# Performance work log

Measured on AMD Instinct MI355X. Metric: run time of the kernel, lower is better.

Reference implementation:

```python
import jax, jax.numpy as jnp
import numpy as np

UNITS = 256

def _lstm_step(carry, idx, kernel, rec_kernel, bias, num_chars):
    h, c = carry
    x = jax.nn.one_hot(idx, num_chars, dtype=h.dtype)          # [B, num_chars]
    z = x @ kernel + h @ rec_kernel + bias                      # [B, 4*UNITS]
    i, f, g, o = jnp.split(z, 4, axis=-1)                       # Keras gate order i,f,c,o
    i = jax.nn.sigmoid(i)
    f = jax.nn.sigmoid(f)
    g = jnp.tanh(g)
    o = jax.nn.sigmoid(o)
    c_new = f * c + i * g
    h_new = o * jnp.tanh(c_new)
    return (h_new, c_new), None


def setup_inputs() -> dict:
    key = jax.random.key(0)
    ks = jax.random.split(key, 4)
    num_chars, batch, seq_len = 128, 1024, 512
    x = jax.random.randint(ks[0], (batch, seq_len), 0, num_chars, dtype=jnp.int32)
    kernel = jax.random.normal(ks[1], (num_chars, 4 * UNITS), dtype=jnp.float32) * 0.05
    rec_kernel = jax.random.normal(ks[2], (UNITS, 4 * UNITS), dtype=jnp.float32) * 0.05
    bias = jnp.zeros((4 * UNITS,), dtype=jnp.float32)
    dense_w = jax.random.normal(ks[3], (UNITS, num_chars), dtype=jnp.float32) * 0.05
    dense_b = jnp.zeros((num_chars,), dtype=jnp.float32)
    return {"x": x, "kernel": kernel, "rec_kernel": rec_kernel, "bias": bias,
            "dense_w": dense_w, "dense_b": dense_b}


def reference(x, kernel, rec_kernel, bias, dense_w, dense_b):
    batch = x.shape[0]
    num_chars = kernel.shape[0]
    h0 = jnp.zeros((batch, UNITS), dtype=kernel.dtype)
    c0 = jnp.zeros((batch, UNITS), dtype=kernel.dtype)
    step = lambda carry, idx: _lstm_step(carry, idx, kernel, rec_kernel, bias, num_chars)
    (h, _), _ = jax.lax.scan(step, (h0, c0), x.T)  # scan over time: [S, B]
    logits = h @ dense_w + dense_b                  # [B, num_chars]
    return jax.nn.softmax(logits, axis=-1)
```

## Files before the change

kernel.cpp:

```cpp
#include <hip/hip_runtime.h>
#include <cstdint>

typedef __bf16 bf16x8 __attribute__((ext_vector_type(8)));
typedef float  f32x4  __attribute__((ext_vector_type(4)));

union U4B { uint4 u; bf16x8 b; };
__device__ __forceinline__ bf16x8 as_bf(uint4 u) { U4B x; x.u = u; return x.b; }

__device__ __forceinline__ unsigned short f2b(float x) {
  unsigned int u = __float_as_uint(x);
  unsigned int r = (u + 0x7fffu + ((u >> 16) & 1u)) >> 16;
  return (unsigned short)r;
}
__device__ __forceinline__ float b2f(unsigned int bits_lo16) {
  return __uint_as_float(bits_lo16 << 16);
}

__device__ __forceinline__ float sigm(float x) {
  float e = __builtin_amdgcn_exp2f(x * -1.4426950408889634f);
  return __builtin_amdgcn_rcpf(1.0f + e);
}
__device__ __forceinline__ float tanh_fast(float x) {
  float e = __builtin_amdgcn_exp2f(x * 2.8853900817779268f);
  return 1.0f - 2.0f * __builtin_amdgcn_rcpf(e + 1.0f);
}

__global__ void prep_kernel(const float* __restrict__ rec,
                            const float* __restrict__ kern,
                            const float* __restrict__ bias,
                            const float* __restrict__ dw,
                            unsigned short* __restrict__ recT,
                            unsigned short* __restrict__ kb2,
                            unsigned short* __restrict__ dwT) {
  int id = blockIdx.x * 256 + threadIdx.x;
  if (id < 262144) {
    int colp = id >> 8, k = id & 255;
    int u = colp >> 2, g = colp & 3;
    recT[colp * 256 + k] = f2b(rec[k * 1024 + u + 256 * g]);
  } else if (id < 262144 + 131072) {
    int i = id - 262144;
    int ch = i >> 10, colp = i & 1023;
    int u = colp >> 2, g = colp & 3;
    int oc = u + 256 * g;
    kb2[ch * 1024 + colp] = f2b(kern[ch * 1024 + oc] + bias[oc]);
  } else {
    int i = id - 262144 - 131072;
    int cls = i >> 8, k = i & 255;
    dwT[cls * 256 + k] = f2b(dw[k * 128 + cls]);
  }
}

__global__ __launch_bounds__(512)
__attribute__((amdgpu_waves_per_eu(2, 2)))
void lstm_kernel(
    const unsigned short* __restrict__ recT,
    const unsigned short* __restrict__ kb2,
    const unsigned short* __restrict__ dwT,
    const int* __restrict__ x,
    const float* __restrict__ dense_b,
    float* __restrict__ out) {
  __shared__ uint4 A_lds[2][8][512];
  __shared__ unsigned short h_buf[2][16][264];

  const int tid   = threadIdx.x;
  const int lane  = tid & 63;
  const int wid   = tid >> 6;
  const int row16 = lane & 15;
  const int kg    = lane >> 4;
  const int rbase = blockIdx.x << 4;

  const unsigned short* recBase = recT + ((wid * 128 + row16) * 256 + kg * 8);

  uint4 af[4][8];
#pragma unroll
  for (int m = 0; m < 4; ++m)
#pragma unroll
    for (int k = 0; k < 8; ++k) {
      af[m][k] = *(const uint4*)(recBase + m * 4096 + k * 32);
      asm volatile("" : "+a"(af[m][k].x), "+a"(af[m][k].y),
                        "+a"(af[m][k].z), "+a"(af[m][k].w));
    }

#pragma unroll
  for (int s = 0; s < 2; ++s)
#pragma unroll
    for (int k = 0; k < 8; ++k)
      A_lds[s][k][wid * 64 + lane] = *(const uint4*)(recBase + (4 + s) * 4096 + k * 32);

  const unsigned short* sb6 = recBase + 6 * 4096;
  const unsigned short* sb7 = recBase + 7 * 4096;
  uint4 st6[8], st7[8];
#pragma unroll
  for (int k = 0; k < 4; ++k) {
    st6[k] = *(const uint4*)(sb6 + k * 32);
    st7[k] = *(const uint4*)(sb7 + k * 32);
  }

  for (int e = tid; e < 16 * 264; e += 512) (&h_buf[0][0][0])[e] = 0;

  float c_state[8];
#pragma unroll
  for (int m = 0; m < 8; ++m) c_state[m] = 0.0f;

  const int* xrow = x + (rbase + row16) * 512;
  int idx_cur = xrow[0];
  const int colb = wid * 128;

  uint2 kq0[4], kq1[4];
  {
    const unsigned short* kb = kb2 + (idx_cur * 1024 + colb + kg * 4);
#pragma unroll
    for (int m = 0; m < 4; ++m) { kq0[m] = *(const uint2*)(kb + m * 16);
                                  kq1[m] = *(const uint2*)(kb + (4 + m) * 16); }
  }

  __syncthreads();

  int cur = 0;
  const unsigned aoff_base = (wid * 64 + lane) * 16;

#pragma unroll 1
  for (int t = 0; t < 512; ++t) {
    unsigned z6 = 0, zL = 0;
    asm volatile("" : "+v"(z6), "+v"(zL));
    const unsigned short* sb6v = sb6 + z6;
    const unsigned short* sb7v = sb7 + z6;
    const unsigned aoff = aoff_base + zL;

#pragma unroll
    for (int k = 4; k < 8; ++k) {
      st6[k] = *(const uint4*)(sb6v + k * 32);
      st7[k] = *(const uint4*)(sb7v + k * 32);
    }
    int idx_next = xrow[(t + 1 < 512) ? t + 1 : 511];

    const unsigned short* hrow = &h_buf[cur][row16][0];
    unsigned short* hn = &h_buf[cur ^ 1][row16][wid * 32 + kg];

    f32x4 a0 = {0,0,0,0}, a1 = {0,0,0,0}, a2 = {0,0,0,0}, a3 = {0,0,0,0};
#pragma unroll
    for (int k = 0; k < 8; ++k) {
      uint4 hf = *(const uint4*)(hrow + k * 32 + kg * 8);
      a0 = __builtin_amdgcn_mfma_f32_16x16x32_bf16(as_bf(af[0][k]), as_bf(hf), a0, 0, 0, 0);
      a1 = __builtin_amdgcn_mfma_f32_16x16x32_bf16(as_bf(af[1][k]), as_bf(hf), a1, 0, 0, 0);
      a2 = __builtin_amdgcn_mfma_f32_16x16x32_bf16(as_bf(af[2][k]), as_bf(hf), a2, 0, 0, 0);
      a3 = __builtin_amdgcn_mfma_f32_16x16x32_bf16(as_bf(af[3][k]), as_bf(hf), a3, 0, 0, 0);
    }
    {
      f32x4 ag[4] = {a0, a1, a2, a3};
#pragma unroll
      for (int m = 0; m < 4; ++m) {
        float zi = ag[m][0] + b2f(kq0[m].x & 0xffffu);
        float zf = ag[m][1] + b2f(kq0[m].x >> 16);
        float zg = ag[m][2] + b2f(kq0[m].y & 0xffffu);
        float zo = ag[m][3] + b2f(kq0[m].y >> 16);
        float c  = sigm(zf) * c_state[m] + sigm(zi) * tanh_fast(zg);
        c_state[m] = c;
        hn[m * 4] = f2b(sigm(zo) * tanh_fast(c));
      }
    }

    const unsigned short* kbn = kb2 + (idx_next * 1024 + colb + kg * 4);
#pragma unroll
    for (int m = 0; m < 4; ++m) kq0[m] = *(const uint2*)(kbn + m * 16);

    f32x4 b0 = {0,0,0,0}, b1 = {0,0,0,0}, b2v = {0,0,0,0}, b3 = {0,0,0,0};
#pragma unroll
    for (int k = 0; k < 8; ++k) {
      uint4 hf = *(const uint4*)(hrow + k * 32 + kg * 8);
      uint4 a4 = *(const uint4*)((const char*)A_lds + (0 * 8 + k) * 8192 + aoff);
      uint4 a5 = *(const uint4*)((const char*)A_lds + (1 * 8 + k) * 8192 + aoff);
      b0 = __builtin_amdgcn_mfma_f32_16x16x32_bf16(as_bf(a4), as_bf(hf), b0, 0, 0, 0);
      b1 = __builtin_amdgcn_mfma_f32_16x16x32_bf16(as_bf(a5), as_bf(hf), b1, 0, 0, 0);
      b2v = __builtin_amdgcn_mfma_f32_16x16x32_bf16(as_bf(st6[k]), as_bf(hf), b2v, 0, 0, 0);
      b3 = __builtin_amdgcn_mfma_f32_16x16x32_bf16(as_bf(st7[k]), as_bf(hf), b3, 0, 0, 0);
      if (k < 4) {
        st6[k] = *(const uint4*)(sb6v + k * 32);
        st7[k] = *(const uint4*)(sb7v + k * 32);
      }
    }
    {
      f32x4 bg[4] = {b0, b1, b2v, b3};
#pragma unroll
      for (int m = 0; m < 4; ++m) {
        float zi = bg[m][0] + b2f(kq1[m].x & 0xffffu);
        float zf = bg[m][1] + b2f(kq1[m].x >> 16);
        float zg = bg[m][2] + b2f(kq1[m].y & 0xffffu);
        float zo = bg[m][3] + b2f(kq1[m].y >> 16);
        float c  = sigm(zf) * c_state[4 + m] + sigm(zi) * tanh_fast(zg);
        c_state[4 + m] = c;
        hn[(4 + m) * 4] = f2b(sigm(zo) * tanh_fast(c));
      }
    }

#pragma unroll
    for (int m = 0; m < 4; ++m) kq1[m] = *(const uint2*)(kbn + (4 + m) * 16);

    __syncthreads();
    cur ^= 1;
    idx_cur = idx_next;
  }

  float (*l_lds)[132] = (float (*)[132])A_lds;
  {
    const unsigned short* dwBase = dwT + ((wid * 16 + row16) * 256 + kg * 8);
    f32x4 la = {0.f, 0.f, 0.f, 0.f};
#pragma unroll
    for (int k = 0; k < 8; ++k) {
      uint4 hf  = *(const uint4*)&h_buf[0][row16][k * 32 + kg * 8];
      uint4 afd = *(const uint4*)(dwBase + k * 32);
      la = __builtin_amdgcn_mfma_f32_16x16x32_bf16(as_bf(afd), as_bf(hf), la, 0, 0, 0);
    }
#pragma unroll
    for (int r = 0; r < 4; ++r) {
      int cls = wid * 16 + kg * 4 + r;
      l_lds[row16][cls] = la[r] + dense_b[cls];
    }
  }
  __syncthreads();

  {
    int r = tid >> 5, cg = tid & 31;
    float4 v = *(const float4*)&l_lds[r][cg * 4];
    float mx = fmaxf(fmaxf(v.x, v.y), fmaxf(v.z, v.w));
#pragma unroll
    for (int sh = 1; sh < 32; sh <<= 1) mx = fmaxf(mx, __shfl_xor(mx, sh));
    const float L2E = 1.4426950408889634f;
    float e0 = __builtin_amdgcn_exp2f((v.x - mx) * L2E);
    float e1 = __builtin_amdgcn_exp2f((v.y - mx) * L2E);
    float e2 = __builtin_amdgcn_exp2f((v.z - mx) * L2E);
    float e3 = __builtin_amdgcn_exp2f((v.w - mx) * L2E);
    float sm = e0 + e1 + e2 + e3;
#pragma unroll
    for (int sh = 1; sh < 32; sh <<= 1) sm += __shfl_xor(sm, sh);
    float inv = __builtin_amdgcn_rcpf(sm);
    float4 o = {e0 * inv, e1 * inv, e2 * inv, e3 * inv};
    *(float4*)&out[(rbase + r) * 128 + cg * 4] = o;
  }
}

extern "C" void kernel_launch(void* const* d_in, const int* in_sizes, int n_in,
                              void* d_out, int out_size, void* d_ws, size_t ws_size,
                              hipStream_t stream) {
  const int*   x      = (const int*)d_in[0];
  const float* kern   = (const float*)d_in[1];
  const float* rec    = (const float*)d_in[2];
  const float* bias   = (const float*)d_in[3];
  const float* dw     = (const float*)d_in[4];
  const float* db     = (const float*)d_in[5];
  float* outp = (float*)d_out;

  unsigned char* ws = (unsigned char*)d_ws;
  unsigned short* recT = (unsigned short*)(ws);
  unsigned short* kb2  = (unsigned short*)(ws + 524288);
  unsigned short* dwT  = (unsigned short*)(ws + 786432);

  prep_kernel<<<1664, 256, 0, stream>>>(rec, kern, bias, dw, recT, kb2, dwT);
  lstm_kernel<<<64, 512, 0, stream>>>(recT, kb2, dwT, x, db, outp);
}
```

Measured before the change: 2.784 ms.

## Permute hidden-unit K order so each lane writes h as one 16-byte store

```diff
diff --git a/kernel.cpp b/kernel.cpp
--- a/kernel.cpp
+++ b/kernel.cpp
@@ -23,6 +23,10 @@
 __device__ __forceinline__ float tanh_fast(float x) {
   float e = __builtin_amdgcn_exp2f(x * 2.8853900817779268f);
   return 1.0f - 2.0f * __builtin_amdgcn_rcpf(e + 1.0f);
+}
+
+__device__ __forceinline__ int kperm_u(int k) {
+  return (k & ~31) + (k & 7) * 4 + ((k >> 3) & 3);
 }
 
 __global__ void prep_kernel(const float* __restrict__ rec,
@@ -35,18 +39,19 @@
   int id = blockIdx.x * 256 + threadIdx.x;
   if (id < 262144) {
     int colp = id >> 8, k = id & 255;
-    int u = colp >> 2, g = colp & 3;
-    recT[colp * 256 + k] = f2b(rec[k * 1024 + u + 256 * g]);
+    int u = kperm_u(k);
+    int oc = (colp >> 2) + 256 * (colp & 3);
+    recT[colp * 256 + k] = f2b(rec[u * 1024 + oc]);
   } else if (id < 262144 + 131072) {
     int i = id - 262144;
     int ch = i >> 10, colp = i & 1023;
-    int u = colp >> 2, g = colp & 3;
-    int oc = u + 256 * g;
+    int oc = (colp >> 2) + 256 * (colp & 3);
     kb2[ch * 1024 + colp] = f2b(kern[ch * 1024 + oc] + bias[oc]);
   } else {
     int i = id - 262144 - 131072;
     int cls = i >> 8, k = i & 255;
-    dwT[cls * 256 + k] = f2b(dw[k * 128 + cls]);
+    int u = kperm_u(k);
+    dwT[cls * 256 + k] = f2b(dw[u * 128 + cls]);
   }
 }
 
@@ -60,7 +65,7 @@
     const float* __restrict__ dense_b,
     float* __restrict__ out) {
   __shared__ uint4 A_lds[2][8][512];
-  __shared__ unsigned short h_buf[2][16][264];
+  __shared__ unsigned short h_buf[2][16][288];
 
   const int tid   = threadIdx.x;
   const int lane  = tid & 63;
@@ -91,12 +96,13 @@
   const unsigned short* sb7 = recBase + 7 * 4096;
   uint4 st6[8], st7[8];
 #pragma unroll
-  for (int k = 0; k < 4; ++k) {
+  for (int k = 0; k < 8; ++k) {
     st6[k] = *(const uint4*)(sb6 + k * 32);
     st7[k] = *(const uint4*)(sb7 + k * 32);
   }
 
-  for (int e = tid; e < 16 * 264; e += 512) (&h_buf[0][0][0])[e] = 0;
+  for (int e = tid; e < 2 * 16 * 288 / 8; e += 512)
+    ((uint4*)h_buf)[e] = uint4{0, 0, 0, 0};
 
   float c_state[8];
 #pragma unroll
@@ -114,11 +120,15 @@
                                   kq1[m] = *(const uint2*)(kb + (4 + m) * 16); }
   }
 
+  char* lds = (char*)&h_buf[0][0][0];
+  const unsigned rowB  = (unsigned)(row16 * 576);
+  const unsigned rdKgo = (unsigned)(kg * 16);
+  const unsigned wrOff = rowB + (unsigned)(wid * 64 + kg * 16);
+  const unsigned aoff_base = (wid * 64 + lane) * 16;
+
   __syncthreads();
 
   int cur = 0;
-  const unsigned aoff_base = (wid * 64 + lane) * 16;
-
 #pragma unroll 1
   for (int t = 0; t < 512; ++t) {
     unsigned z6 = 0, zL = 0;
@@ -127,26 +137,21 @@
     const unsigned short* sb7v = sb7 + z6;
     const unsigned aoff = aoff_base + zL;
 
-#pragma unroll
-    for (int k = 4; k < 8; ++k) {
-      st6[k] = *(const uint4*)(sb6v + k * 32);
-      st7[k] = *(const uint4*)(sb7v + k * 32);
-    }
     int idx_next = xrow[(t + 1 < 512) ? t + 1 : 511];
 
-    const unsigned short* hrow = &h_buf[cur][row16][0];
-    unsigned short* hn = &h_buf[cur ^ 1][row16][wid * 32 + kg];
-
-    f32x4 a0 = {0,0,0,0}, a1 = {0,0,0,0}, a2 = {0,0,0,0}, a3 = {0,0,0,0};
-#pragma unroll
-    for (int k = 0; k < 8; ++k) {
-      uint4 hf = *(const uint4*)(hrow + k * 32 + kg * 8);
-      a0 = __builtin_amdgcn_mfma_f32_16x16x32_bf16(as_bf(af[0][k]), as_bf(hf), a0, 0, 0, 0);
-      a1 = __builtin_amdgcn_mfma_f32_16x16x32_bf16(as_bf(af[1][k]), as_bf(hf), a1, 0, 0, 0);
-      a2 = __builtin_amdgcn_mfma_f32_16x16x32_bf16(as_bf(af[2][k]), as_bf(hf), a2, 0, 0, 0);
-      a3 = __builtin_amdgcn_mfma_f32_16x16x32_bf16(as_bf(af[3][k]), as_bf(hf), a3, 0, 0, 0);
-    }
+    const char* hrdRow = lds + cur * 9216 + rowB;
+    unsigned short hb[8];
+
     {
+      f32x4 a0 = {0,0,0,0}, a1 = {0,0,0,0}, a2 = {0,0,0,0}, a3 = {0,0,0,0};
+#pragma unroll
+      for (int k = 0; k < 8; ++k) {
+        uint4 hf = *(const uint4*)(hrdRow + k * 64 + rdKgo);
+        a0 = __builtin_amdgcn_mfma_f32_16x16x32_bf16(as_bf(af[0][k]), as_bf(hf), a0, 0, 0, 0);
+        a1 = __builtin_amdgcn_mfma_f32_16x16x32_bf16(as_bf(af[1][k]), as_bf(hf), a1, 0, 0, 0);
+        a2 = __builtin_amdgcn_mfma_f32_16x16x32_bf16(as_bf(af[2][k]), as_bf(hf), a2, 0, 0, 0);
+        a3 = __builtin_amdgcn_mfma_f32_16x16x32_bf16(as_bf(af[3][k]), as_bf(hf), a3, 0, 0, 0);
+      }
       f32x4 ag[4] = {a0, a1, a2, a3};
 #pragma unroll
       for (int m = 0; m < 4; ++m) {
@@ -156,7 +161,7 @@
         float zo = ag[m][3] + b2f(kq0[m].y >> 16);
         float c  = sigm(zf) * c_state[m] + sigm(zi) * tanh_fast(zg);
         c_state[m] = c;
-        hn[m * 4] = f2b(sigm(zo) * tanh_fast(c));
+        hb[m] = f2b(sigm(zo) * tanh_fast(c));
       }
     }
 
@@ -164,22 +169,20 @@
 #pragma unroll
     for (int m = 0; m < 4; ++m) kq0[m] = *(const uint2*)(kbn + m * 16);
 
-    f32x4 b0 = {0,0,0,0}, b1 = {0,0,0,0}, b2v = {0,0,0,0}, b3 = {0,0,0,0};
-#pragma unroll
-    for (int k = 0; k < 8; ++k) {
-      uint4 hf = *(const uint4*)(hrow + k * 32 + kg * 8);
-      uint4 a4 = *(const uint4*)((const char*)A_lds + (0 * 8 + k) * 8192 + aoff);
-      uint4 a5 = *(const uint4*)((const char*)A_lds + (1 * 8 + k) * 8192 + aoff);
-      b0 = __builtin_amdgcn_mfma_f32_16x16x32_bf16(as_bf(a4), as_bf(hf), b0, 0, 0, 0);
-      b1 = __builtin_amdgcn_mfma_f32_16x16x32_bf16(as_bf(a5), as_bf(hf), b1, 0, 0, 0);
-      b2v = __builtin_amdgcn_mfma_f32_16x16x32_bf16(as_bf(st6[k]), as_bf(hf), b2v, 0, 0, 0);
-      b3 = __builtin_amdgcn_mfma_f32_16x16x32_bf16(as_bf(st7[k]), as_bf(hf), b3, 0, 0, 0);
-      if (k < 4) {
+    {
+      f32x4 b0 = {0,0,0,0}, b1 = {0,0,0,0}, b2v = {0,0,0,0}, b3 = {0,0,0,0};
+#pragma unroll
+      for (int k = 0; k < 8; ++k) {
+        uint4 hf = *(const uint4*)(hrdRow + k * 64 + rdKgo);
+        uint4 a4 = *(const uint4*)((const char*)A_lds + (0 * 8 + k) * 8192 + aoff);
+        uint4 a5 = *(const uint4*)((const char*)A_lds + (1 * 8 + k) * 8192 + aoff);
+        b0  = __builtin_amdgcn_mfma_f32_16x16x32_bf16(as_bf(a4), as_bf(hf), b0, 0, 0, 0);
+        b1  = __builtin_amdgcn_mfma_f32_16x16x32_bf16(as_bf(a5), as_bf(hf), b1, 0, 0, 0);
+        b2v = __builtin_amdgcn_mfma_f32_16x16x32_bf16(as_bf(st6[k]), as_bf(hf), b2v, 0, 0, 0);
+        b3  = __builtin_amdgcn_mfma_f32_16x16x32_bf16(as_bf(st7[k]), as_bf(hf), b3, 0, 0, 0);
         st6[k] = *(const uint4*)(sb6v + k * 32);
         st7[k] = *(const uint4*)(sb7v + k * 32);
       }
-    }
-    {
       f32x4 bg[4] = {b0, b1, b2v, b3};
 #pragma unroll
       for (int m = 0; m < 4; ++m) {
@@ -189,14 +192,23 @@
         float zo = bg[m][3] + b2f(kq1[m].y >> 16);
         float c  = sigm(zf) * c_state[4 + m] + sigm(zi) * tanh_fast(zg);
         c_state[4 + m] = c;
-        hn[(4 + m) * 4] = f2b(sigm(zo) * tanh_fast(c));
+        hb[4 + m] = f2b(sigm(zo) * tanh_fast(c));
       }
     }
 
 #pragma unroll
     for (int m = 0; m < 4; ++m) kq1[m] = *(const uint2*)(kbn + (4 + m) * 16);
 
-    __syncthreads();
+    uint4 hwv;
+    hwv.x = (unsigned)hb[0] | ((unsigned)hb[1] << 16);
+    hwv.y = (unsigned)hb[2] | ((unsigned)hb[3] << 16);
+    hwv.z = (unsigned)hb[4] | ((unsigned)hb[5] << 16);
+    hwv.w = (unsigned)hb[6] | ((unsigned)hb[7] << 16);
+    *(uint4*)(lds + (cur ^ 1) * 9216 + wrOff) = hwv;
+
+    asm volatile("s_waitcnt lgkmcnt(0)" ::: "memory");
+    __builtin_amdgcn_s_barrier();
+
     cur ^= 1;
     idx_cur = idx_next;
   }
@@ -207,10 +219,11 @@
     f32x4 la = {0.f, 0.f, 0.f, 0.f};
 #pragma unroll
     for (int k = 0; k < 8; ++k) {
-      uint4 hf  = *(const uint4*)&h_buf[0][row16][k * 32 + kg * 8];
+      uint4 hf  = *(const uint4*)(lds + rowB + k * 64 + rdKgo);
       uint4 afd = *(const uint4*)(dwBase + k * 32);
       la = __builtin_amdgcn_mfma_f32_16x16x32_bf16(as_bf(afd), as_bf(hf), la, 0, 0, 0);
     }
+    __syncthreads();
 #pragma unroll
     for (int r = 0; r < 4; ++r) {
       int cls = wid * 16 + kg * 4 + r;
```

After: 4.082 ms. 46.6% more time.

## Stage input-gate rows through LDS and stream three recurrent slices from global

Applied to the files above, without the earlier changes.

```diff
diff --git a/kernel.cpp b/kernel.cpp
--- a/kernel.cpp
+++ b/kernel.cpp
@@ -59,7 +59,8 @@
     const int* __restrict__ x,
     const float* __restrict__ dense_b,
     float* __restrict__ out) {
-  __shared__ uint4 A_lds[2][8][512];
+  __shared__ uint4 A_lds[8][512];
+  __shared__ unsigned short kq_lds[2][16][1032];
   __shared__ unsigned short h_buf[2][16][264];
 
   const int tid   = threadIdx.x;
@@ -82,16 +83,16 @@
     }
 
 #pragma unroll
-  for (int s = 0; s < 2; ++s)
-#pragma unroll
-    for (int k = 0; k < 8; ++k)
-      A_lds[s][k][wid * 64 + lane] = *(const uint4*)(recBase + (4 + s) * 4096 + k * 32);
-
+  for (int k = 0; k < 8; ++k)
+    A_lds[k][wid * 64 + lane] = *(const uint4*)(recBase + 4 * 4096 + k * 32);
+
+  const unsigned short* sb5 = recBase + 5 * 4096;
   const unsigned short* sb6 = recBase + 6 * 4096;
   const unsigned short* sb7 = recBase + 7 * 4096;
-  uint4 st6[8], st7[8];
-#pragma unroll
-  for (int k = 0; k < 4; ++k) {
+  uint4 st5[2], st6[2], st7[2];
+#pragma unroll
+  for (int k = 0; k < 2; ++k) {
+    st5[k] = *(const uint4*)(sb5 + k * 32);
     st6[k] = *(const uint4*)(sb6 + k * 32);
     st7[k] = *(const uint4*)(sb7 + k * 32);
   }
@@ -102,17 +103,23 @@
 #pragma unroll
   for (int m = 0; m < 8; ++m) c_state[m] = 0.0f;
 
-  const int* xrow = x + (rbase + row16) * 512;
-  int idx_cur = xrow[0];
-  const int colb = wid * 128;
-
-  uint2 kq0[4], kq1[4];
+  const int r0 = 2 * wid, r1 = 2 * wid + 1;
   {
-    const unsigned short* kb = kb2 + (idx_cur * 1024 + colb + kg * 4);
-#pragma unroll
-    for (int m = 0; m < 4; ++m) { kq0[m] = *(const uint2*)(kb + m * 16);
-                                  kq1[m] = *(const uint2*)(kb + (4 + m) * 16); }
-  }
+    int ia0 = x[(rbase + r0) * 512 + 0];
+    int ia1 = x[(rbase + r1) * 512 + 0];
+    const unsigned short* s0 = kb2 + ia0 * 1024;
+    const unsigned short* s1 = kb2 + ia1 * 1024;
+    uint4 a = *(const uint4*)(s0 + lane * 8);
+    uint4 b = *(const uint4*)(s0 + 512 + lane * 8);
+    uint4 c = *(const uint4*)(s1 + lane * 8);
+    uint4 d = *(const uint4*)(s1 + 512 + lane * 8);
+    *(uint4*)((char*)&kq_lds[0][r0][0] + lane * 16) = a;
+    *(uint4*)((char*)&kq_lds[0][r0][0] + 1024 + lane * 16) = b;
+    *(uint4*)((char*)&kq_lds[0][r1][0] + lane * 16) = c;
+    *(uint4*)((char*)&kq_lds[0][r1][0] + 1024 + lane * 16) = d;
+  }
+  int ib0 = x[(rbase + r0) * 512 + 1];
+  int ib1 = x[(rbase + r1) * 512 + 1];
 
   __syncthreads();
 
@@ -123,82 +130,89 @@
   for (int t = 0; t < 512; ++t) {
     unsigned z6 = 0, zL = 0;
     asm volatile("" : "+v"(z6), "+v"(zL));
+    const unsigned short* sb5v = sb5 + z6;
     const unsigned short* sb6v = sb6 + z6;
     const unsigned short* sb7v = sb7 + z6;
     const unsigned aoff = aoff_base + zL;
 
-#pragma unroll
-    for (int k = 4; k < 8; ++k) {
-      st6[k] = *(const uint4*)(sb6v + k * 32);
-      st7[k] = *(const uint4*)(sb7v + k * 32);
-    }
-    int idx_next = xrow[(t + 1 < 512) ? t + 1 : 511];
-
-    const unsigned short* hrow = &h_buf[cur][row16][0];
-    unsigned short* hn = &h_buf[cur ^ 1][row16][wid * 32 + kg];
-
-    f32x4 a0 = {0,0,0,0}, a1 = {0,0,0,0}, a2 = {0,0,0,0}, a3 = {0,0,0,0};
-#pragma unroll
-    for (int k = 0; k < 8; ++k) {
-      uint4 hf = *(const uint4*)(hrow + k * 32 + kg * 8);
-      a0 = __builtin_amdgcn_mfma_f32_16x16x32_bf16(as_bf(af[0][k]), as_bf(hf), a0, 0, 0, 0);
-      a1 = __builtin_amdgcn_mfma_f32_16x16x32_bf16(as_bf(af[1][k]), as_bf(hf), a1, 0, 0, 0);
-      a2 = __builtin_amdgcn_mfma_f32_16x16x32_bf16(as_bf(af[2][k]), as_bf(hf), a2, 0, 0, 0);
-      a3 = __builtin_amdgcn_mfma_f32_16x16x32_bf16(as_bf(af[3][k]), as_bf(hf), a3, 0, 0, 0);
-    }
+    const unsigned short* s0 = kb2 + ib0 * 1024;
+    const unsigned short* s1 = kb2 + ib1 * 1024;
+    uint4 q0 = *(const uint4*)(s0 + lane * 8);
+    uint4 q1 = *(const uint4*)(s0 + 512 + lane * 8);
+    uint4 q2 = *(const uint4*)(s1 + lane * 8);
+    uint4 q3 = *(const uint4*)(s1 + 512 + lane * 8);
+    int tn2 = (t + 2 < 512) ? t + 2 : 511;
+    ib0 = x[(rbase + r0) * 512 + tn2];
+    ib1 = x[(rbase + r1) * 512 + tn2];
+
+    const unsigned short* hrow  = &h_buf[cur][row16][0];
+    unsigned short*       hn    = &h_buf[cur ^ 1][row16][wid * 32 + kg];
+    const unsigned short* kqrow = &kq_lds[cur][row16][wid * 128 + kg * 4];
+
     {
+      f32x4 a0 = {0,0,0,0}, a1 = {0,0,0,0}, a2 = {0,0,0,0}, a3 = {0,0,0,0};
+#pragma unroll
+      for (int k = 0; k < 8; ++k) {
+        uint4 hf = *(const uint4*)(hrow + k * 32 + kg * 8);
+        a0 = __builtin_amdgcn_mfma_f32_16x16x32_bf16(as_bf(af[0][k]), as_bf(hf), a0, 0, 0, 0);
+        a1 = __builtin_amdgcn_mfma_f32_16x16x32_bf16(as_bf(af[1][k]), as_bf(hf), a1, 0, 0, 0);
+        a2 = __builtin_amdgcn_mfma_f32_16x16x32_bf16(as_bf(af[2][k]), as_bf(hf), a2, 0, 0, 0);
+        a3 = __builtin_amdgcn_mfma_f32_16x16x32_bf16(as_bf(af[3][k]), as_bf(hf), a3, 0, 0, 0);
+      }
       f32x4 ag[4] = {a0, a1, a2, a3};
 #pragma unroll
       for (int m = 0; m < 4; ++m) {
-        float zi = ag[m][0] + b2f(kq0[m].x & 0xffffu);
-        float zf = ag[m][1] + b2f(kq0[m].x >> 16);
-        float zg = ag[m][2] + b2f(kq0[m].y & 0xffffu);
-        float zo = ag[m][3] + b2f(kq0[m].y >> 16);
+        uint2 kq = *(const uint2*)(kqrow + m * 16);
+        float zi = ag[m][0] + b2f(kq.x & 0xffffu);
+        float zf = ag[m][1] + b2f(kq.x >> 16);
+        float zg = ag[m][2] + b2f(kq.y & 0xffffu);
+        float zo = ag[m][3] + b2f(kq.y >> 16);
         float c  = sigm(zf) * c_state[m] + sigm(zi) * tanh_fast(zg);
         c_state[m] = c;
         hn[m * 4] = f2b(sigm(zo) * tanh_fast(c));
       }
     }
 
-    const unsigned short* kbn = kb2 + (idx_next * 1024 + colb + kg * 4);
-#pragma unroll
-    for (int m = 0; m < 4; ++m) kq0[m] = *(const uint2*)(kbn + m * 16);
-
-    f32x4 b0 = {0,0,0,0}, b1 = {0,0,0,0}, b2v = {0,0,0,0}, b3 = {0,0,0,0};
-#pragma unroll
-    for (int k = 0; k < 8; ++k) {
-      uint4 hf = *(const uint4*)(hrow + k * 32 + kg * 8);
-      uint4 a4 = *(const uint4*)((const char*)A_lds + (0 * 8 + k) * 8192 + aoff);
-      uint4 a5 = *(const uint4*)((const char*)A_lds + (1 * 8 + k) * 8192 + aoff);
-      b0 = __builtin_amdgcn_mfma_f32_16x16x32_bf16(as_bf(a4), as_bf(hf), b0, 0, 0, 0);
-      b1 = __builtin_amdgcn_mfma_f32_16x16x32_bf16(as_bf(a5), as_bf(hf), b1, 0, 0, 0);
-      b2v = __builtin_amdgcn_mfma_f32_16x16x32_bf16(as_bf(st6[k]), as_bf(hf), b2v, 0, 0, 0);
-      b3 = __builtin_amdgcn_mfma_f32_16x16x32_bf16(as_bf(st7[k]), as_bf(hf), b3, 0, 0, 0);
-      if (k < 4) {
-        st6[k] = *(const uint4*)(sb6v + k * 32);
-        st7[k] = *(const uint4*)(sb7v + k * 32);
-      }
-    }
     {
+      char* qd0 = (char*)&kq_lds[cur ^ 1][r0][0];
+      char* qd1 = (char*)&kq_lds[cur ^ 1][r1][0];
+      *(uint4*)(qd0 + lane * 16) = q0;
+      *(uint4*)(qd0 + 1024 + lane * 16) = q1;
+      *(uint4*)(qd1 + lane * 16) = q2;
+      *(uint4*)(qd1 + 1024 + lane * 16) = q3;
+    }
+
+    {
+      f32x4 b0 = {0,0,0,0}, b1 = {0,0,0,0}, b2v = {0,0,0,0}, b3 = {0,0,0,0};
+#pragma unroll
+      for (int k = 0; k < 8; ++k) {
+        uint4 hf = *(const uint4*)(hrow + k * 32 + kg * 8);
+        uint4 a4 = *(const uint4*)((const char*)A_lds + k * 8192 + aoff);
+        b0  = __builtin_amdgcn_mfma_f32_16x16x32_bf16(as_bf(a4), as_bf(hf), b0, 0, 0, 0);
+        b1  = __builtin_amdgcn_mfma_f32_16x16x32_bf16(as_bf(st5[k & 1]), as_bf(hf), b1, 0, 0, 0);
+        b2v = __builtin_amdgcn_mfma_f32_16x16x32_bf16(as_bf(st6[k & 1]), as_bf(hf), b2v, 0, 0, 0);
+        b3  = __builtin_amdgcn_mfma_f32_16x16x32_bf16(as_bf(st7[k & 1]), as_bf(hf), b3, 0, 0, 0);
+        const int kp = (k + 2) & 7;
+        st5[k & 1] = *(const uint4*)(sb5v + kp * 32);
+        st6[k & 1] = *(const uint4*)(sb6v + kp * 32);
+        st7[k & 1] = *(const uint4*)(sb7v + kp * 32);
+      }
       f32x4 bg[4] = {b0, b1, b2v, b3};
 #pragma unroll
       for (int m = 0; m < 4; ++m) {
-        float zi = bg[m][0] + b2f(kq1[m].x & 0xffffu);
-        float zf = bg[m][1] + b2f(kq1[m].x >> 16);
-        float zg = bg[m][2] + b2f(kq1[m].y & 0xffffu);
-        float zo = bg[m][3] + b2f(kq1[m].y >> 16);
+        uint2 kq = *(const uint2*)(kqrow + (4 + m) * 16);
+        float zi = bg[m][0] + b2f(kq.x & 0xffffu);
+        float zf = bg[m][1] + b2f(kq.x >> 16);
+        float zg = bg[m][2] + b2f(kq.y & 0xffffu);
+        float zo = bg[m][3] + b2f(kq.y >> 16);
         float c  = sigm(zf) * c_state[4 + m] + sigm(zi) * tanh_fast(zg);
         c_state[4 + m] = c;
         hn[(4 + m) * 4] = f2b(sigm(zo) * tanh_fast(c));
       }
     }
 
-#pragma unroll
-    for (int m = 0; m < 4; ++m) kq1[m] = *(const uint2*)(kbn + (4 + m) * 16);
-
     __syncthreads();
     cur ^= 1;
-    idx_cur = idx_next;
   }
 
   float (*l_lds)[132] = (float (*)[132])A_lds;
@@ -211,6 +225,7 @@
       uint4 afd = *(const uint4*)(dwBase + k * 32);
       la = __builtin_amdgcn_mfma_f32_16x16x32_bf16(as_bf(afd), as_bf(hf), la, 0, 0, 0);
     }
+    __syncthreads();
 #pragma unroll
     for (int r = 0; r < 4; ++r) {
       int cls = wid * 16 + kg * 4 + r;
```

Result: slower. 3.289 ms (+18.1%).
